# Kernel optimization log

Measured on AMD Instinct MI355X. Metric: run time of the kernel, lower is better.

Reference implementation:

```python
import jax, jax.numpy as jnp
import numpy as np

ALPHA = 0.01  # leaky_relu slope (forward default)

def _hist_entropy(x, bins):
    """Mean over batch of per-sample histogram entropy, matching
    np.histogram(sample, bins=bins) + entropy_calc(hist, bw=bins):
      H = -sum(p*log(p)) - log(1/bins) = -sum(p*log(p)) + log(bins).
    x: [B, D] float."""
    B, D = x.shape
    xmin = jnp.min(x, axis=1, keepdims=True)
    xmax = jnp.max(x, axis=1, keepdims=True)
    width = xmax - xmin
    safe_w = jnp.where(width > 0, width, 1.0)
    # np.histogram: equal-width bins over [min, max]; max value goes in last bin
    idx = jnp.floor((x - xmin) / safe_w * bins).astype(jnp.int32)
    idx = jnp.clip(idx, 0, bins - 1)
    flat = (jnp.arange(B, dtype=jnp.int32)[:, None] * bins + idx).reshape(-1)
    counts = jnp.zeros(B * bins, jnp.float32).at[flat].add(1.0).reshape(B, bins)
    p = counts / jnp.float32(D)
    plogp = jnp.where(p > 0, p * jnp.log(jnp.where(p > 0, p, 1.0)), 0.0)
    H = -jnp.sum(plogp, axis=1) + jnp.log(jnp.float32(bins))  # [B]
    return jnp.mean(H)

def _lin(x, W, b):
    return x @ W.T + b

def setup_inputs() -> dict:
    key = jax.random.key(0)
    ks = jax.random.split(key, 13)
    B = 65536
    dims = [(784, 256), (256, 128), (128, 128), (128, 128), (128, 32), (32, 10)]
    inp = {"x": jax.random.normal(ks[0], (B, 784), dtype=jnp.float32)}
    for i, (din, dout) in enumerate(dims):
        s = 1.0 / np.sqrt(din)
        inp[f"W{i+1}"] = jax.random.uniform(ks[1 + 2 * i], (dout, din), jnp.float32, -s, s)
        inp[f"b{i+1}"] = jax.random.uniform(ks[2 + 2 * i], (dout,), jnp.float32, -s, s)
    return inp

def reference(x, W1, b1, W2, b2, W3, b3, W4, b4, W5, b5, W6, b6):
    x = x.reshape(-1, 784)
    Hs = []
    for (W, b) in [(W1, b1), (W2, b2), (W3, b3), (W4, b4), (W5, b5)]:
        x = jax.nn.leaky_relu(_lin(x, W, b), ALPHA)
        Hs.append(_hist_entropy(x, x.shape[1]))  # bins = dim / bin_ratio(=1)
    x = jax.nn.relu(_lin(x, W6, b6))
    out = jax.nn.log_softmax(x, axis=1)
    return (out, Hs[0], Hs[1], Hs[2], Hs[3], Hs[4])
```

## Files before the change

### kernel.cpp

```cpp
#include <hip/hip_runtime.h>
#include <hip/hip_bf16.h>
#include <math.h>

#define ALPHA 0.01f

typedef __bf16 bf16x8 __attribute__((ext_vector_type(8)));
typedef float  floatx4 __attribute__((ext_vector_type(4)));

static __device__ __forceinline__ unsigned short f2bf_bits(float f) {
    return __builtin_bit_cast(unsigned short, (__bf16)f);
}

static __device__ __forceinline__ void glds16(const void* g, void* l) {
    __builtin_amdgcn_global_load_lds(
        (const __attribute__((address_space(1))) unsigned int*)g,
        (__attribute__((address_space(3))) unsigned int*)l, 16, 0, 0);
}

template <int CTRL>
static __device__ __forceinline__ float dppmov(float x) {
    int r = __builtin_amdgcn_update_dpp(0, __builtin_bit_cast(int, x), CTRL, 0xf, 0xf, false);
    return __builtin_bit_cast(float, r);
}
static __device__ __forceinline__ float red16min(float x) {
    x = fminf(x, dppmov<0x121>(x)); x = fminf(x, dppmov<0x122>(x));
    x = fminf(x, dppmov<0x124>(x)); x = fminf(x, dppmov<0x128>(x));
    return x;
}
static __device__ __forceinline__ float red16max(float x) {
    x = fmaxf(x, dppmov<0x121>(x)); x = fmaxf(x, dppmov<0x122>(x));
    x = fmaxf(x, dppmov<0x124>(x)); x = fmaxf(x, dppmov<0x128>(x));
    return x;
}
static __device__ __forceinline__ float red16sum(float x) {
    x += dppmov<0x121>(x); x += dppmov<0x122>(x);
    x += dppmov<0x124>(x); x += dppmov<0x128>(x);
    return x;
}

template <int DIN, int DOUT, bool XF32, bool WRES, int MINB>
__global__ __launch_bounds__(256, MINB) void layer_mfma(
    const void* __restrict__ Xin, const unsigned short* __restrict__ Wf,
    const float* __restrict__ bias, unsigned short* __restrict__ Y,
    float* __restrict__ Hpart)
{
    constexpr int CTN     = DOUT / 16;
    constexpr int KT_FULL = DIN / 32;
    constexpr int TAIL    = DIN % 32;
    constexpr int HALF    = DOUT / 2;
    constexpr int LOG2D   = (DOUT == 256) ? 8 : (DOUT == 128) ? 7 : 5;
    constexpr float LOGB  = (DOUT == 256) ? 5.54517744f
                          : (DOUT == 128) ? 4.85203026f : 3.46573590f;
    constexpr int XBYTES  = WRES ? 16 : 64 * 32 * (XF32 ? 4 : 2);
    constexpr int WBYTES  = WRES ? (size_t)DIN * DOUT * 2 : DOUT * 64;
    constexpr int WSLOTS  = (DIN / 32) * CTN * 64;
    static_assert(DOUT % 32 == 0 && DOUT <= 256, "DOUT");
    static_assert(XF32 || TAIL == 0, "bf16 input requires DIN%32==0");

    __shared__ __align__(16) char smemX[XBYTES];
    __shared__ __align__(16) char smemW[WBYTES];
    __shared__ unsigned int counts[16][HALF + 1];
    __shared__ float hsum[4];

    const int t      = threadIdx.x;
    const int lane   = t & 63;
    const int lane16 = lane & 15;
    const int q      = lane >> 4;
    const int w      = t >> 6;
    const int row0   = blockIdx.x * 64;
    const int myrow  = w * 16 + lane16;

    float biasr[CTN];
    #pragma unroll
    for (int ct = 0; ct < CTN; ct++) biasr[ct] = bias[ct * 16 + lane16];

    floatx4 acc[CTN];
    #pragma unroll
    for (int ct = 0; ct < CTN; ct++) acc[ct] = (floatx4)(0.0f);

    if constexpr (WRES) {
        static_assert(WSLOTS % 256 == 0, "WSLOTS");
        #pragma unroll
        for (int i = 0; i < WSLOTS / 256; i++)
            glds16(Wf + ((size_t)(i * 256 + w * 64 + lane)) * 8,
                   smemW + (i * 256 + w * 64) * 16);
        __syncthreads();

        const unsigned short* X = (const unsigned short*)Xin;
        const size_t abase = (size_t)(row0 + myrow) * DIN + q * 8;
        bf16x8 acur = *(const bf16x8*)(X + abase);
        #pragma unroll
        for (int kt = 0; kt < KT_FULL; kt++) {
            bf16x8 anxt = acur;
            if (kt + 1 < KT_FULL)
                anxt = *(const bf16x8*)(X + abase + (kt + 1) * 32);
            #pragma unroll
            for (int ct = 0; ct < CTN; ct++) {
                bf16x8 bw = *(const bf16x8*)(smemW + ((kt * CTN + ct) * 64 + lane) * 16);
                acc[ct] = __builtin_amdgcn_mfma_f32_16x16x32_bf16(acur, bw, acc[ct], 0, 0, 0);
            }
            acur = anxt;
        }
    } else {
        auto stageW = [&](int kt) {
            #pragma unroll
            for (int j = w; j < CTN; j += 4)
                glds16(Wf + ((size_t)kt * CTN * 64 + j * 64 + lane) * 8,
                       smemW + j * 64 * 16);
        };
        auto stageX = [&](int kt) {
            const float* X = (const float*)Xin;
            #pragma unroll
            for (int j = 0; j < 2; j++) {
                int s  = w * 128 + j * 64 + lane;
                int gc = (s & ~7) | ((s ^ (s >> 3)) & 7);
                int r  = gc >> 3, c = gc & 7;
                glds16(X + (size_t)(row0 + r) * DIN + kt * 32 + c * 4,
                       smemX + (w * 128 + j * 64) * 16);
            }
        };
        auto compute = [&]() {
            int s0 = myrow * 8 + (((2 * q)     ^ myrow) & 7);
            int s1 = myrow * 8 + (((2 * q + 1) ^ myrow) & 7);
            float4 f0 = *(const float4*)(smemX + s0 * 16);
            float4 f1 = *(const float4*)(smemX + s1 * 16);
            uint4 pk;
            pk.x = (unsigned)f2bf_bits(f0.x) | ((unsigned)f2bf_bits(f0.y) << 16);
            pk.y = (unsigned)f2bf_bits(f0.z) | ((unsigned)f2bf_bits(f0.w) << 16);
            pk.z = (unsigned)f2bf_bits(f1.x) | ((unsigned)f2bf_bits(f1.y) << 16);
            pk.w = (unsigned)f2bf_bits(f1.z) | ((unsigned)f2bf_bits(f1.w) << 16);
            bf16x8 a = __builtin_bit_cast(bf16x8, pk);
            #pragma unroll
            for (int ct = 0; ct < CTN; ct++) {
                bf16x8 bw = *(const bf16x8*)(smemW + (ct * 64 + lane) * 16);
                acc[ct] = __builtin_amdgcn_mfma_f32_16x16x32_bf16(a, bw, acc[ct], 0, 0, 0);
            }
        };

        #pragma unroll 1
        for (int kt = 0; kt < KT_FULL; kt++) {
            __syncthreads();
            stageX(kt);
            stageW(kt);
            __syncthreads();
            compute();
        }
        if constexpr (TAIL > 0) {
            __syncthreads();
            stageW(KT_FULL);
            {
                const float* X = (const float*)Xin;
                int r = t >> 2, c = t & 3;
                float4 v = *(const float4*)(X + (size_t)(row0 + r) * DIN
                                            + KT_FULL * 32 + c * 4);
                *(float4*)(smemX + (r * 8 + ((c ^ r) & 7)) * 16) = v;
                int c2 = c + 4;
                *(float4*)(smemX + (r * 8 + ((c2 ^ r) & 7)) * 16)
                    = make_float4(0.f, 0.f, 0.f, 0.f);
            }
            __syncthreads();
            compute();
        }
    }

    #pragma unroll
    for (int ct = 0; ct < CTN; ct++) {
        #pragma unroll
        for (int reg = 0; reg < 4; reg++) {
            float v = acc[ct][reg] + biasr[ct];
            v = v > 0.0f ? v : ALPHA * v;
            acc[ct][reg] = v;
            Y[(size_t)(row0 + w * 16 + q * 4 + reg) * DOUT
              + ct * 16 + lane16] = f2bf_bits(v);
        }
    }

    unsigned int* cc = counts[w * 4 + q];
    float Hq = 0.0f;
    #pragma unroll
    for (int reg = 0; reg < 4; reg++) {
        float mn = acc[0][reg], mx = mn;
        #pragma unroll
        for (int ct = 1; ct < CTN; ct++) {
            mn = fminf(mn, acc[ct][reg]);
            mx = fmaxf(mx, acc[ct][reg]);
        }
        mn = red16min(mn);
        mx = red16max(mx);
        float wdt = mx - mn;
        float scale = (float)DOUT / (wdt > 0.0f ? wdt : 1.0f);

        #pragma unroll
        for (int i = 0; i < DOUT / 32; i++) cc[lane16 + 16 * i] = 0u;

        #pragma unroll
        for (int ct = 0; ct < CTN; ct++) {
            int b = (int)((acc[ct][reg] - mn) * scale);
            b = b < (DOUT - 1) ? b : (DOUT - 1);
            atomicAdd(&cc[b & (HALF - 1)],
                      1u << (((b >> (LOG2D - 1)) & 1) << 4));
        }

        float s = 0.0f;
        #pragma unroll
        for (int i = 0; i < DOUT / 32; i++) {
            unsigned int word = cc[lane16 + 16 * i];
            int c0 = (int)(word & 0xffffu), c1 = (int)(word >> 16);
            if (c0 > 0) { float p = (float)c0 * (1.0f / (float)DOUT); s += p * __logf(p); }
            if (c1 > 0) { float p = (float)c1 * (1.0f / (float)DOUT); s += p * __logf(p); }
        }
        s = red16sum(s);
        Hq += LOGB - s;
    }
    Hq += __shfl_xor(Hq, 16, 64);
    Hq += __shfl_xor(Hq, 32, 64);

    if (lane == 0) hsum[w] = Hq;
    __syncthreads();
    if (t == 0) Hpart[blockIdx.x] = hsum[0] + hsum[1] + hsum[2] + hsum[3];
}

template <int DIN, int DOUT, bool AG>
static __device__ __forceinline__ float tail_layer(
    const unsigned short* __restrict__ Ag, size_t arow,
    char* __restrict__ yt,
    const unsigned short* __restrict__ Wf, const float* __restrict__ bias,
    unsigned int* __restrict__ cc, int lane)
{
    constexpr int KT  = DIN / 32, CTN = DOUT / 16;
    constexpr int NCI = DIN / 8,  NCO = DOUT / 8;
    constexpr int HALF  = DOUT / 2;
    constexpr int LOG2D = (DOUT == 128) ? 7 : 5;
    constexpr float LOGB = (DOUT == 128) ? 4.85203026f : 3.46573590f;
    const int lane16 = lane & 15, q = lane >> 4;

    bf16x8 a[KT];
    if constexpr (AG) {
        #pragma unroll
        for (int kt = 0; kt < KT; kt++)
            a[kt] = *(const bf16x8*)(Ag + arow + q * 8 + kt * 32);
    } else {
        asm volatile("s_waitcnt lgkmcnt(0)" ::: "memory");
        #pragma unroll
        for (int kt = 0; kt < KT; kt++) {
            int cs = (kt * 4 + q) ^ (lane16 & (NCI - 1));
            a[kt] = *(const bf16x8*)(yt + lane16 * (DIN * 2) + cs * 16);
        }
    }

    float biasr[CTN];
    #pragma unroll
    for (int ct = 0; ct < CTN; ct++) biasr[ct] = bias[ct * 16 + lane16];

    floatx4 acc[CTN];
    #pragma unroll
    for (int ct = 0; ct < CTN; ct++) acc[ct] = (floatx4)(0.0f);

    #pragma unroll
    for (int kt = 0; kt < KT; kt++) {
        #pragma unroll
        for (int ct = 0; ct < CTN; ct++) {
            bf16x8 bw = *(const bf16x8*)(Wf + ((size_t)(kt * CTN + ct) * 64 + lane) * 8);
            acc[ct] = __builtin_amdgcn_mfma_f32_16x16x32_bf16(a[kt], bw, acc[ct], 0, 0, 0);
        }
    }

    #pragma unroll
    for (int ct = 0; ct < CTN; ct++) {
        #pragma unroll
        for (int reg = 0; reg < 4; reg++) {
            float v = acc[ct][reg] + biasr[ct];
            v = v > 0.0f ? v : ALPHA * v;
            acc[ct][reg] = v;
            int r  = q * 4 + reg;
            int c  = (ct * 16 + lane16) >> 3;
            int cs = c ^ (r & (NCO - 1));
            *(unsigned short*)(yt + r * (DOUT * 2) + cs * 16 + (lane16 & 7) * 2)
                = f2bf_bits(v);
        }
    }

    float Hq = 0.0f;
    #pragma unroll
    for (int reg = 0; reg < 4; reg++) {
        float mn = acc[0][reg], mx = mn;
        #pragma unroll
        for (int ct = 1; ct < CTN; ct++) {
            mn = fminf(mn, acc[ct][reg]);
            mx = fmaxf(mx, acc[ct][reg]);
        }
        mn = red16min(mn);
        mx = red16max(mx);
        float wdt = mx - mn;
        float scale = (float)DOUT / (wdt > 0.0f ? wdt : 1.0f);

        #pragma unroll
        for (int i = 0; i < DOUT / 32; i++) cc[lane16 + 16 * i] = 0u;

        #pragma unroll
        for (int ct = 0; ct < CTN; ct++) {
            int b = (int)((acc[ct][reg] - mn) * scale);
            b = b < (DOUT - 1) ? b : (DOUT - 1);
            atomicAdd(&cc[b & (HALF - 1)],
                      1u << (((b >> (LOG2D - 1)) & 1) << 4));
        }

        float s = 0.0f;
        #pragma unroll
        for (int i = 0; i < DOUT / 32; i++) {
            unsigned int word = cc[lane16 + 16 * i];
            int c0 = (int)(word & 0xffffu), c1 = (int)(word >> 16);
            if (c0 > 0) { float p = (float)c0 * (1.0f / (float)DOUT); s += p * __logf(p); }
            if (c1 > 0) { float p = (float)c1 * (1.0f / (float)DOUT); s += p * __logf(p); }
        }
        s = red16sum(s);
        Hq += LOGB - s;
    }
    Hq += __shfl_xor(Hq, 16, 64);
    Hq += __shfl_xor(Hq, 32, 64);
    return Hq;
}

__global__ __launch_bounds__(256, 3) void tail_fused(
    const unsigned short* __restrict__ Xb,
    const unsigned short* __restrict__ W2f, const float* __restrict__ b2,
    const unsigned short* __restrict__ W3f, const float* __restrict__ b3,
    const unsigned short* __restrict__ W4f, const float* __restrict__ b4,
    const unsigned short* __restrict__ W5f, const float* __restrict__ b5,
    const float* __restrict__ W6, const float* __restrict__ b6,
    float* __restrict__ out, float* __restrict__ Hpart)
{
    __shared__ __align__(16) char yts[4][16 * 128 * 2];
    __shared__ unsigned int counts[16][65];

    const int t = threadIdx.x;
    const int lane = t & 63, lane16 = lane & 15, q = lane >> 4, w = t >> 6;
    char* yt = yts[w];
    unsigned int* cc = counts[w * 4 + q];
    const int row0 = blockIdx.x * 64 + w * 16;
    const size_t arow = (size_t)(row0 + lane16) * 256;
    const int hidx = blockIdx.x * 4 + w;

    float H;
    H = tail_layer<256, 128, true >(Xb, arow, yt, W2f, b2, cc, lane);
    if (lane == 0) Hpart[1 * 4096 + hidx] = H;
    H = tail_layer<128, 128, false>(Xb, 0, yt, W3f, b3, cc, lane);
    if (lane == 0) Hpart[2 * 4096 + hidx] = H;
    H = tail_layer<128, 128, false>(Xb, 0, yt, W4f, b4, cc, lane);
    if (lane == 0) Hpart[3 * 4096 + hidx] = H;
    H = tail_layer<128,  32, false>(Xb, 0, yt, W5f, b5, cc, lane);
    if (lane == 0) Hpart[4 * 4096 + hidx] = H;

    asm volatile("s_waitcnt lgkmcnt(0)" ::: "memory");
    float x[32];
    #pragma unroll
    for (int c = 0; c < 4; c++) {
        int cs = c ^ (lane16 & 3);
        bf16x8 v = *(const bf16x8*)(yt + lane16 * 64 + cs * 16);
        #pragma unroll
        for (int j = 0; j < 8; j++) x[c * 8 + j] = (float)v[j];
    }

    float z[3];
    float m = -1e30f;
    #pragma unroll
    for (int s2 = 0; s2 < 3; s2++) {
        int jj = q * 3 + s2;
        float a6 = 0.0f;
        if (jj < 10) {
            a6 = b6[jj];
            #pragma unroll
            for (int k = 0; k < 32; k++) a6 = fmaf(x[k], W6[jj * 32 + k], a6);
            a6 = fmaxf(a6, 0.0f);
            m = fmaxf(m, a6);
        }
        z[s2] = a6;
    }
    m = fmaxf(m, __shfl_xor(m, 16, 64));
    m = fmaxf(m, __shfl_xor(m, 32, 64));
    float se = 0.0f;
    #pragma unroll
    for (int s2 = 0; s2 < 3; s2++)
        if (q * 3 + s2 < 10) se += __expf(z[s2] - m);
    se += __shfl_xor(se, 16, 64);
    se += __shfl_xor(se, 32, 64);
    float ls = __logf(se);
    const size_t ro = (size_t)(row0 + lane16) * 10;
    #pragma unroll
    for (int s2 = 0; s2 < 3; s2++) {
        int jj = q * 3 + s2;
        if (jj < 10) out[ro + jj] = z[s2] - m - ls;
    }
}

__global__ void convert_wfrag(const float* __restrict__ W1, const float* __restrict__ W2,
                              const float* __restrict__ W3, const float* __restrict__ W4,
                              const float* __restrict__ W5, unsigned short* __restrict__ out)
{
    int s = blockIdx.x * 256 + threadIdx.x;
    if (s >= 34304) return;
    const float* W; int DIN, CTN, sl;
    if      (s < 25600) { W = W1; DIN = 784; CTN = 16; sl = s;         }
    else if (s < 29696) { W = W2; DIN = 256; CTN = 8;  sl = s - 25600; }
    else if (s < 31744) { W = W3; DIN = 128; CTN = 8;  sl = s - 29696; }
    else if (s < 33792) { W = W4; DIN = 128; CTN = 8;  sl = s - 31744; }
    else                { W = W5; DIN = 128; CTN = 2;  sl = s - 33792; }
    int kt = sl / (CTN * 64);
    int ct = (sl / 64) % CTN;
    int ln = sl & 63;
    int r  = ct * 16 + (ln & 15);
    int k0 = kt * 32 + (ln >> 4) * 8;
    unsigned short v[8];
    #pragma unroll
    for (int j = 0; j < 8; j++) {
        int k = k0 + j;
        v[j] = (k < DIN) ? f2bf_bits(W[(size_t)r * DIN + k]) : (unsigned short)0;
    }
    uint4 pk;
    pk.x = (unsigned)v[0] | ((unsigned)v[1] << 16);
    pk.y = (unsigned)v[2] | ((unsigned)v[3] << 16);
    pk.z = (unsigned)v[4] | ((unsigned)v[5] << 16);
    pk.w = (unsigned)v[6] | ((unsigned)v[7] << 16);
    *(uint4*)(out + (size_t)s * 8) = pk;
}

__global__ __launch_bounds__(256) void hreduce(const float* __restrict__ Hp,
                                               float* __restrict__ out_tail)
{
    __shared__ float sm[4];
    const int t = threadIdx.x, lane = t & 63, w = t >> 6;
    const int l = blockIdx.x;
    const int n = l ? 4096 : 1024;
    const float* p = Hp + (size_t)l * 4096;
    float s = 0.0f;
    for (int i = t; i < n; i += 256) s += p[i];
    #pragma unroll
    for (int off = 1; off <= 32; off <<= 1) s += __shfl_xor(s, off, 64);
    if (lane == 0) sm[w] = s;
    __syncthreads();
    if (t == 0)
        out_tail[l] = (sm[0] + sm[1] + sm[2] + sm[3]) * (1.0f / 65536.0f);
}

extern "C" void kernel_launch(void* const* d_in, const int* in_sizes, int n_in,
                              void* d_out, int out_size, void* d_ws, size_t ws_size,
                              hipStream_t stream)
{
    const float* x  = (const float*)d_in[0];
    const float* W1 = (const float*)d_in[1];  const float* b1 = (const float*)d_in[2];
    const float* W2 = (const float*)d_in[3];  const float* b2 = (const float*)d_in[4];
    const float* W3 = (const float*)d_in[5];  const float* b3 = (const float*)d_in[6];
    const float* W4 = (const float*)d_in[7];  const float* b4 = (const float*)d_in[8];
    const float* W5 = (const float*)d_in[9];  const float* b5 = (const float*)d_in[10];
    const float* W6 = (const float*)d_in[11]; const float* b6 = (const float*)d_in[12];
    float* out = (float*)d_out;

    constexpr int B = 65536;
    char* ws = (char*)d_ws;
    float* Hpart = (float*)ws;
    unsigned short* Wfrag = (unsigned short*)(ws + 81920);
    unsigned short* W1f = Wfrag;
    unsigned short* W2f = W1f + 25600 * 8;
    unsigned short* W3f = W2f + 4096 * 8;
    unsigned short* W4f = W3f + 2048 * 8;
    unsigned short* W5f = W4f + 2048 * 8;
    unsigned short* bufA = (unsigned short*)(ws + (1 << 20));

    convert_wfrag<<<134, 256, 0, stream>>>(W1, W2, W3, W4, W5, Wfrag);

    layer_mfma<784, 256, true, false, 4><<<B / 64, 256, 0, stream>>>(
        x, W1f, b1, bufA, Hpart);

    tail_fused<<<B / 64, 256, 0, stream>>>(
        bufA, W2f, b2, W3f, b3, W4f, b4, W5f, b5, W6, b6, out, Hpart);

    hreduce<<<5, 256, 0, stream>>>(Hpart, out + (size_t)B * 10);
}
```

Measured before the change: 408.4 us.

## Fuse layer-1 GEMM with tail layers into one mega kernel

Measured after the change: 401.6 us. About the same (-1.7%).

```diff
diff --git a/kernel.cpp b/kernel.cpp
--- a/kernel.cpp
+++ b/kernel.cpp
@@ -9,6 +9,9 @@
 
 static __device__ __forceinline__ unsigned short f2bf_bits(float f) {
     return __builtin_bit_cast(unsigned short, (__bf16)f);
+}
+static __device__ __forceinline__ float bf2f(unsigned short u) {
+    return __builtin_bit_cast(float, (unsigned)u << 16);
 }
 
 static __device__ __forceinline__ void glds16(const void* g, void* l) {
@@ -38,78 +41,146 @@
     return x;
 }
 
-template <int DIN, int DOUT, bool XF32, bool WRES, int MINB>
-__global__ __launch_bounds__(256, MINB) void layer_mfma(
-    const void* __restrict__ Xin, const unsigned short* __restrict__ Wf,
-    const float* __restrict__ bias, unsigned short* __restrict__ Y,
-    float* __restrict__ Hpart)
-{
-    constexpr int CTN     = DOUT / 16;
-    constexpr int KT_FULL = DIN / 32;
-    constexpr int TAIL    = DIN % 32;
-    constexpr int HALF    = DOUT / 2;
-    constexpr int LOG2D   = (DOUT == 256) ? 8 : (DOUT == 128) ? 7 : 5;
-    constexpr float LOGB  = (DOUT == 256) ? 5.54517744f
-                          : (DOUT == 128) ? 4.85203026f : 3.46573590f;
-    constexpr int XBYTES  = WRES ? 16 : 64 * 32 * (XF32 ? 4 : 2);
-    constexpr int WBYTES  = WRES ? (size_t)DIN * DOUT * 2 : DOUT * 64;
-    constexpr int WSLOTS  = (DIN / 32) * CTN * 64;
-    static_assert(DOUT % 32 == 0 && DOUT <= 256, "DOUT");
-    static_assert(XF32 || TAIL == 0, "bf16 input requires DIN%32==0");
-
-    __shared__ __align__(16) char smemX[XBYTES];
-    __shared__ __align__(16) char smemW[WBYTES];
-    __shared__ unsigned int counts[16][HALF + 1];
+template <int DOUT>
+static __device__ __forceinline__ float entropy_tile(const floatx4* acc,
+        unsigned int* cc, int lane16)
+{
+    constexpr int CTN   = DOUT / 16;
+    constexpr int HALF  = DOUT / 2;
+    constexpr int LOG2D = (DOUT == 256) ? 8 : (DOUT == 128) ? 7 : 5;
+    constexpr float LOGB = (DOUT == 256) ? 5.54517744f
+                         : (DOUT == 128) ? 4.85203026f : 3.46573590f;
+    float Hq = 0.0f;
+    #pragma unroll
+    for (int reg = 0; reg < 4; reg++) {
+        float mn = acc[0][reg], mx = mn;
+        #pragma unroll
+        for (int ct = 1; ct < CTN; ct++) {
+            mn = fminf(mn, acc[ct][reg]);
+            mx = fmaxf(mx, acc[ct][reg]);
+        }
+        mn = red16min(mn);
+        mx = red16max(mx);
+        float wdt = mx - mn;
+        float scale = (float)DOUT / (wdt > 0.0f ? wdt : 1.0f);
+
+        #pragma unroll
+        for (int i = 0; i < DOUT / 32; i++) cc[lane16 + 16 * i] = 0u;
+
+        #pragma unroll
+        for (int ct = 0; ct < CTN; ct++) {
+            int b = (int)((acc[ct][reg] - mn) * scale);
+            b = b < (DOUT - 1) ? b : (DOUT - 1);
+            atomicAdd(&cc[b & (HALF - 1)],
+                      1u << (((b >> (LOG2D - 1)) & 1) << 4));
+        }
+
+        float s = 0.0f;
+        #pragma unroll
+        for (int i = 0; i < DOUT / 32; i++) {
+            unsigned int word = cc[lane16 + 16 * i];
+            int c0 = (int)(word & 0xffffu), c1 = (int)(word >> 16);
+            if (c0 > 0) { float p = (float)c0 * (1.0f / (float)DOUT); s += p * __logf(p); }
+            if (c1 > 0) { float p = (float)c1 * (1.0f / (float)DOUT); s += p * __logf(p); }
+        }
+        s = red16sum(s);
+        Hq += LOGB - s;
+    }
+    Hq += __shfl_xor(Hq, 16, 64);
+    Hq += __shfl_xor(Hq, 32, 64);
+    return Hq;
+}
+
+template <int DIN, int DOUT>
+static __device__ __forceinline__ float tail_layer(const bf16x8* a,
+    char* __restrict__ yt,
+    const unsigned short* __restrict__ Wf, const float* __restrict__ bias,
+    unsigned int* __restrict__ cc, int lane)
+{
+    constexpr int KT = DIN / 32, CTN = DOUT / 16, NCO = DOUT / 8;
+    const int lane16 = lane & 15, q = lane >> 4;
+
+    floatx4 acc[CTN];
+    #pragma unroll
+    for (int ct = 0; ct < CTN; ct++) acc[ct] = (floatx4)(0.0f);
+
+    #pragma unroll
+    for (int kt = 0; kt < KT; kt++) {
+        #pragma unroll
+        for (int ct = 0; ct < CTN; ct++) {
+            bf16x8 bw = *(const bf16x8*)(Wf + ((size_t)(kt * CTN + ct) * 64 + lane) * 8);
+            acc[ct] = __builtin_amdgcn_mfma_f32_16x16x32_bf16(a[kt], bw, acc[ct], 0, 0, 0);
+        }
+    }
+
+    #pragma unroll
+    for (int ct = 0; ct < CTN; ct++) {
+        float bb = bias[ct * 16 + lane16];
+        #pragma unroll
+        for (int reg = 0; reg < 4; reg++) {
+            float v = acc[ct][reg] + bb;
+            v = v > 0.0f ? v : ALPHA * v;
+            acc[ct][reg] = v;
+            int r  = q * 4 + reg;
+            int c  = (ct * 16 + lane16) >> 3;
+            int cs = c ^ (r & (NCO - 1));
+            *(unsigned short*)(yt + r * (DOUT * 2) + cs * 16 + (lane16 & 7) * 2)
+                = f2bf_bits(v);
+        }
+    }
+    return entropy_tile<DOUT>(acc, cc, lane16);
+}
+
+template <int DIN>
+static __device__ __forceinline__ void load_afrags(bf16x8* a,
+    const char* __restrict__ yt, int lane16, int q)
+{
+    constexpr int KT = DIN / 32, NCI = DIN / 8;
+    asm volatile("s_waitcnt lgkmcnt(0)" ::: "memory");
+    #pragma unroll
+    for (int kt = 0; kt < KT; kt++) {
+        int cs = (kt * 4 + q) ^ (lane16 & (NCI - 1));
+        a[kt] = *(const bf16x8*)(yt + lane16 * (DIN * 2) + cs * 16);
+    }
+    asm volatile("s_waitcnt lgkmcnt(0)" ::: "memory");
+}
+
+__global__ __launch_bounds__(256, 4) void mega(
+    const float* __restrict__ X,
+    const unsigned short* __restrict__ W1f, const float* __restrict__ b1,
+    const unsigned short* __restrict__ W2f, const float* __restrict__ b2,
+    const unsigned short* __restrict__ W3f, const float* __restrict__ b3,
+    const unsigned short* __restrict__ W4f, const float* __restrict__ b4,
+    const unsigned short* __restrict__ W5f, const float* __restrict__ b5,
+    const float* __restrict__ W6, const float* __restrict__ b6,
+    float* __restrict__ out, float* __restrict__ Hpart)
+{
+    __shared__ __align__(16) char regA[24576];
+    __shared__ unsigned int cnt[16][129];
     __shared__ float hsum[4];
 
-    const int t      = threadIdx.x;
-    const int lane   = t & 63;
-    const int lane16 = lane & 15;
-    const int q      = lane >> 4;
-    const int w      = t >> 6;
-    const int row0   = blockIdx.x * 64;
-    const int myrow  = w * 16 + lane16;
-
-    float biasr[CTN];
-    #pragma unroll
-    for (int ct = 0; ct < CTN; ct++) biasr[ct] = bias[ct * 16 + lane16];
-
-    floatx4 acc[CTN];
-    #pragma unroll
-    for (int ct = 0; ct < CTN; ct++) acc[ct] = (floatx4)(0.0f);
-
-    if constexpr (WRES) {
-        static_assert(WSLOTS % 256 == 0, "WSLOTS");
-        #pragma unroll
-        for (int i = 0; i < WSLOTS / 256; i++)
-            glds16(Wf + ((size_t)(i * 256 + w * 64 + lane)) * 8,
-                   smemW + (i * 256 + w * 64) * 16);
-        __syncthreads();
-
-        const unsigned short* X = (const unsigned short*)Xin;
-        const size_t abase = (size_t)(row0 + myrow) * DIN + q * 8;
-        bf16x8 acur = *(const bf16x8*)(X + abase);
-        #pragma unroll
-        for (int kt = 0; kt < KT_FULL; kt++) {
-            bf16x8 anxt = acur;
-            if (kt + 1 < KT_FULL)
-                anxt = *(const bf16x8*)(X + abase + (kt + 1) * 32);
-            #pragma unroll
-            for (int ct = 0; ct < CTN; ct++) {
-                bf16x8 bw = *(const bf16x8*)(smemW + ((kt * CTN + ct) * 64 + lane) * 16);
-                acc[ct] = __builtin_amdgcn_mfma_f32_16x16x32_bf16(acur, bw, acc[ct], 0, 0, 0);
-            }
-            acur = anxt;
-        }
-    } else {
+    const int t = threadIdx.x;
+    const int lane = t & 63, lane16 = lane & 15, q = lane >> 4, w = t >> 6;
+    const int row0 = blockIdx.x * 64;
+    const int myrow = w * 16 + lane16;
+    unsigned int* cc = cnt[w * 4 + q];
+    char* yt = regA + w * 4096;
+
+    floatx4 acc1[16];
+    #pragma unroll
+    for (int ct = 0; ct < 16; ct++) acc1[ct] = (floatx4)(0.0f);
+    {
+        constexpr int DIN = 784, CTN = 16, KT_FULL = 24;
+        char* smemX = regA;
+        char* smemW = regA + 8192;
+
         auto stageW = [&](int kt) {
             #pragma unroll
             for (int j = w; j < CTN; j += 4)
-                glds16(Wf + ((size_t)kt * CTN * 64 + j * 64 + lane) * 8,
+                glds16(W1f + ((size_t)kt * CTN * 64 + j * 64 + lane) * 8,
                        smemW + j * 64 * 16);
         };
         auto stageX = [&](int kt) {
-            const float* X = (const float*)Xin;
             #pragma unroll
             for (int j = 0; j < 2; j++) {
                 int s  = w * 128 + j * 64 + lane;
@@ -133,7 +204,7 @@
             #pragma unroll
             for (int ct = 0; ct < CTN; ct++) {
                 bf16x8 bw = *(const bf16x8*)(smemW + (ct * 64 + lane) * 16);
-                acc[ct] = __builtin_amdgcn_mfma_f32_16x16x32_bf16(a, bw, acc[ct], 0, 0, 0);
+                acc1[ct] = __builtin_amdgcn_mfma_f32_16x16x32_bf16(a, bw, acc1[ct], 0, 0, 0);
             }
         };
 
@@ -145,220 +216,83 @@
             __syncthreads();
             compute();
         }
-        if constexpr (TAIL > 0) {
-            __syncthreads();
-            stageW(KT_FULL);
-            {
-                const float* X = (const float*)Xin;
-                int r = t >> 2, c = t & 3;
-                float4 v = *(const float4*)(X + (size_t)(row0 + r) * DIN
-                                            + KT_FULL * 32 + c * 4);
-                *(float4*)(smemX + (r * 8 + ((c ^ r) & 7)) * 16) = v;
-                int c2 = c + 4;
-                *(float4*)(smemX + (r * 8 + ((c2 ^ r) & 7)) * 16)
-                    = make_float4(0.f, 0.f, 0.f, 0.f);
-            }
-            __syncthreads();
-            compute();
-        }
-    }
-
-    #pragma unroll
-    for (int ct = 0; ct < CTN; ct++) {
+        __syncthreads();
+        stageW(KT_FULL);
+        {
+            int r = t >> 2, c = t & 3;
+            float4 v = *(const float4*)(X + (size_t)(row0 + r) * DIN
+                                        + KT_FULL * 32 + c * 4);
+            *(float4*)(smemX + (r * 8 + ((c ^ r) & 7)) * 16) = v;
+            int c2 = c + 4;
+            *(float4*)(smemX + (r * 8 + ((c2 ^ r) & 7)) * 16)
+                = make_float4(0.f, 0.f, 0.f, 0.f);
+        }
+        __syncthreads();
+        compute();
+    }
+
+    #pragma unroll
+    for (int ct = 0; ct < 16; ct++) {
+        float bb = b1[ct * 16 + lane16];
         #pragma unroll
         for (int reg = 0; reg < 4; reg++) {
-            float v = acc[ct][reg] + biasr[ct];
-            v = v > 0.0f ? v : ALPHA * v;
-            acc[ct][reg] = v;
-            Y[(size_t)(row0 + w * 16 + q * 4 + reg) * DOUT
-              + ct * 16 + lane16] = f2bf_bits(v);
-        }
-    }
-
-    unsigned int* cc = counts[w * 4 + q];
-    float Hq = 0.0f;
-    #pragma unroll
-    for (int reg = 0; reg < 4; reg++) {
-        float mn = acc[0][reg], mx = mn;
-        #pragma unroll
-        for (int ct = 1; ct < CTN; ct++) {
-            mn = fminf(mn, acc[ct][reg]);
-            mx = fmaxf(mx, acc[ct][reg]);
-        }
-        mn = red16min(mn);
-        mx = red16max(mx);
-        float wdt = mx - mn;
-        float scale = (float)DOUT / (wdt > 0.0f ? wdt : 1.0f);
-
-        #pragma unroll
-        for (int i = 0; i < DOUT / 32; i++) cc[lane16 + 16 * i] = 0u;
-
-        #pragma unroll
-        for (int ct = 0; ct < CTN; ct++) {
-            int b = (int)((acc[ct][reg] - mn) * scale);
-            b = b < (DOUT - 1) ? b : (DOUT - 1);
-            atomicAdd(&cc[b & (HALF - 1)],
-                      1u << (((b >> (LOG2D - 1)) & 1) << 4));
-        }
-
-        float s = 0.0f;
-        #pragma unroll
-        for (int i = 0; i < DOUT / 32; i++) {
-            unsigned int word = cc[lane16 + 16 * i];
-            int c0 = (int)(word & 0xffffu), c1 = (int)(word >> 16);
-            if (c0 > 0) { float p = (float)c0 * (1.0f / (float)DOUT); s += p * __logf(p); }
-            if (c1 > 0) { float p = (float)c1 * (1.0f / (float)DOUT); s += p * __logf(p); }
-        }
-        s = red16sum(s);
-        Hq += LOGB - s;
-    }
-    Hq += __shfl_xor(Hq, 16, 64);
-    Hq += __shfl_xor(Hq, 32, 64);
-
-    if (lane == 0) hsum[w] = Hq;
+            float v = acc1[ct][reg] + bb;
+            acc1[ct][reg] = v > 0.0f ? v : ALPHA * v;
+        }
+    }
+
+    float H1 = entropy_tile<256>(acc1, cc, lane16);
+    if (lane == 0) hsum[w] = H1;
     __syncthreads();
     if (t == 0) Hpart[blockIdx.x] = hsum[0] + hsum[1] + hsum[2] + hsum[3];
-}
-
-template <int DIN, int DOUT, bool AG>
-static __device__ __forceinline__ float tail_layer(
-    const unsigned short* __restrict__ Ag, size_t arow,
-    char* __restrict__ yt,
-    const unsigned short* __restrict__ Wf, const float* __restrict__ bias,
-    unsigned int* __restrict__ cc, int lane)
-{
-    constexpr int KT  = DIN / 32, CTN = DOUT / 16;
-    constexpr int NCI = DIN / 8,  NCO = DOUT / 8;
-    constexpr int HALF  = DOUT / 2;
-    constexpr int LOG2D = (DOUT == 128) ? 7 : 5;
-    constexpr float LOGB = (DOUT == 128) ? 4.85203026f : 3.46573590f;
-    const int lane16 = lane & 15, q = lane >> 4;
-
-    bf16x8 a[KT];
-    if constexpr (AG) {
-        #pragma unroll
-        for (int kt = 0; kt < KT; kt++)
-            a[kt] = *(const bf16x8*)(Ag + arow + q * 8 + kt * 32);
-    } else {
+
+    bf16x8 a2[8];
+    #pragma unroll
+    for (int p = 0; p < 2; p++) {
+        #pragma unroll
+        for (int ct = 0; ct < 8; ct++) {
+            #pragma unroll
+            for (int reg = 0; reg < 4; reg++) {
+                int r  = q * 4 + reg;
+                int c  = (ct * 16 + lane16) >> 3;
+                int cs = c ^ r;
+                *(unsigned short*)(yt + r * 256 + cs * 16 + (lane16 & 7) * 2)
+                    = f2bf_bits(acc1[p * 8 + ct][reg]);
+            }
+        }
         asm volatile("s_waitcnt lgkmcnt(0)" ::: "memory");
         #pragma unroll
-        for (int kt = 0; kt < KT; kt++) {
-            int cs = (kt * 4 + q) ^ (lane16 & (NCI - 1));
-            a[kt] = *(const bf16x8*)(yt + lane16 * (DIN * 2) + cs * 16);
-        }
-    }
-
-    float biasr[CTN];
-    #pragma unroll
-    for (int ct = 0; ct < CTN; ct++) biasr[ct] = bias[ct * 16 + lane16];
-
-    floatx4 acc[CTN];
-    #pragma unroll
-    for (int ct = 0; ct < CTN; ct++) acc[ct] = (floatx4)(0.0f);
-
-    #pragma unroll
-    for (int kt = 0; kt < KT; kt++) {
-        #pragma unroll
-        for (int ct = 0; ct < CTN; ct++) {
-            bf16x8 bw = *(const bf16x8*)(Wf + ((size_t)(kt * CTN + ct) * 64 + lane) * 8);
-            acc[ct] = __builtin_amdgcn_mfma_f32_16x16x32_bf16(a[kt], bw, acc[ct], 0, 0, 0);
-        }
-    }
-
-    #pragma unroll
-    for (int ct = 0; ct < CTN; ct++) {
-        #pragma unroll
-        for (int reg = 0; reg < 4; reg++) {
-            float v = acc[ct][reg] + biasr[ct];
-            v = v > 0.0f ? v : ALPHA * v;
-            acc[ct][reg] = v;
-            int r  = q * 4 + reg;
-            int c  = (ct * 16 + lane16) >> 3;
-            int cs = c ^ (r & (NCO - 1));
-            *(unsigned short*)(yt + r * (DOUT * 2) + cs * 16 + (lane16 & 7) * 2)
-                = f2bf_bits(v);
-        }
-    }
-
-    float Hq = 0.0f;
-    #pragma unroll
-    for (int reg = 0; reg < 4; reg++) {
-        float mn = acc[0][reg], mx = mn;
-        #pragma unroll
-        for (int ct = 1; ct < CTN; ct++) {
-            mn = fminf(mn, acc[ct][reg]);
-            mx = fmaxf(mx, acc[ct][reg]);
-        }
-        mn = red16min(mn);
-        mx = red16max(mx);
-        float wdt = mx - mn;
-        float scale = (float)DOUT / (wdt > 0.0f ? wdt : 1.0f);
-
-        #pragma unroll
-        for (int i = 0; i < DOUT / 32; i++) cc[lane16 + 16 * i] = 0u;
-
-        #pragma unroll
-        for (int ct = 0; ct < CTN; ct++) {
-            int b = (int)((acc[ct][reg] - mn) * scale);
-            b = b < (DOUT - 1) ? b : (DOUT - 1);
-            atomicAdd(&cc[b & (HALF - 1)],
-                      1u << (((b >> (LOG2D - 1)) & 1) << 4));
-        }
-
-        float s = 0.0f;
-        #pragma unroll
-        for (int i = 0; i < DOUT / 32; i++) {
-            unsigned int word = cc[lane16 + 16 * i];
-            int c0 = (int)(word & 0xffffu), c1 = (int)(word >> 16);
-            if (c0 > 0) { float p = (float)c0 * (1.0f / (float)DOUT); s += p * __logf(p); }
-            if (c1 > 0) { float p = (float)c1 * (1.0f / (float)DOUT); s += p * __logf(p); }
-        }
-        s = red16sum(s);
-        Hq += LOGB - s;
-    }
-    Hq += __shfl_xor(Hq, 16, 64);
-    Hq += __shfl_xor(Hq, 32, 64);
-    return Hq;
-}
-
-__global__ __launch_bounds__(256, 3) void tail_fused(
-    const unsigned short* __restrict__ Xb,
-    const unsigned short* __restrict__ W2f, const float* __restrict__ b2,
-    const unsigned short* __restrict__ W3f, const float* __restrict__ b3,
-    const unsigned short* __restrict__ W4f, const float* __restrict__ b4,
-    const unsigned short* __restrict__ W5f, const float* __restrict__ b5,
-    const float* __restrict__ W6, const float* __restrict__ b6,
-    float* __restrict__ out, float* __restrict__ Hpart)
-{
-    __shared__ __align__(16) char yts[4][16 * 128 * 2];
-    __shared__ unsigned int counts[16][65];
-
-    const int t = threadIdx.x;
-    const int lane = t & 63, lane16 = lane & 15, q = lane >> 4, w = t >> 6;
-    char* yt = yts[w];
-    unsigned int* cc = counts[w * 4 + q];
-    const int row0 = blockIdx.x * 64 + w * 16;
-    const size_t arow = (size_t)(row0 + lane16) * 256;
-    const int hidx = blockIdx.x * 4 + w;
-
-    float H;
-    H = tail_layer<256, 128, true >(Xb, arow, yt, W2f, b2, cc, lane);
-    if (lane == 0) Hpart[1 * 4096 + hidx] = H;
-    H = tail_layer<128, 128, false>(Xb, 0, yt, W3f, b3, cc, lane);
-    if (lane == 0) Hpart[2 * 4096 + hidx] = H;
-    H = tail_layer<128, 128, false>(Xb, 0, yt, W4f, b4, cc, lane);
-    if (lane == 0) Hpart[3 * 4096 + hidx] = H;
-    H = tail_layer<128,  32, false>(Xb, 0, yt, W5f, b5, cc, lane);
-    if (lane == 0) Hpart[4 * 4096 + hidx] = H;
+        for (int kt = 0; kt < 4; kt++) {
+            int cs = (kt * 4 + q) ^ lane16;
+            a2[p * 4 + kt] = *(const bf16x8*)(yt + lane16 * 256 + cs * 16);
+        }
+        asm volatile("s_waitcnt lgkmcnt(0)" ::: "memory");
+    }
+
+    float H = tail_layer<256, 128>(a2, yt, W2f, b2, cc, lane);
+    if (lane == 0) Hpart[1 * 4096 + blockIdx.x * 4 + w] = H;
+
+    bf16x8 a[4];
+    load_afrags<128>(a, yt, lane16, q);
+    H = tail_layer<128, 128>(a, yt, W3f, b3, cc, lane);
+    if (lane == 0) Hpart[2 * 4096 + blockIdx.x * 4 + w] = H;
+
+    load_afrags<128>(a, yt, lane16, q);
+    H = tail_layer<128, 128>(a, yt, W4f, b4, cc, lane);
+    if (lane == 0) Hpart[3 * 4096 + blockIdx.x * 4 + w] = H;
+
+    load_afrags<128>(a, yt, lane16, q);
+    H = tail_layer<128, 32>(a, yt, W5f, b5, cc, lane);
+    if (lane == 0) Hpart[4 * 4096 + blockIdx.x * 4 + w] = H;
 
     asm volatile("s_waitcnt lgkmcnt(0)" ::: "memory");
-    float x[32];
+    float x6[32];
     #pragma unroll
     for (int c = 0; c < 4; c++) {
         int cs = c ^ (lane16 & 3);
         bf16x8 v = *(const bf16x8*)(yt + lane16 * 64 + cs * 16);
         #pragma unroll
-        for (int j = 0; j < 8; j++) x[c * 8 + j] = (float)v[j];
+        for (int j = 0; j < 8; j++) x6[c * 8 + j] = (float)v[j];
     }
 
     float z[3];
@@ -370,7 +304,7 @@
         if (jj < 10) {
             a6 = b6[jj];
             #pragma unroll
-            for (int k = 0; k < 32; k++) a6 = fmaf(x[k], W6[jj * 32 + k], a6);
+            for (int k = 0; k < 32; k++) a6 = fmaf(x6[k], W6[jj * 32 + k], a6);
             a6 = fmaxf(a6, 0.0f);
             m = fmaxf(m, a6);
         }
@@ -385,7 +319,7 @@
     se += __shfl_xor(se, 16, 64);
     se += __shfl_xor(se, 32, 64);
     float ls = __logf(se);
-    const size_t ro = (size_t)(row0 + lane16) * 10;
+    const size_t ro = (size_t)(row0 + w * 16 + lane16) * 10;
     #pragma unroll
     for (int s2 = 0; s2 < 3; s2++) {
         int jj = q * 3 + s2;
@@ -464,15 +398,11 @@
     unsigned short* W3f = W2f + 4096 * 8;
     unsigned short* W4f = W3f + 2048 * 8;
     unsigned short* W5f = W4f + 2048 * 8;
-    unsigned short* bufA = (unsigned short*)(ws + (1 << 20));
 
     convert_wfrag<<<134, 256, 0, stream>>>(W1, W2, W3, W4, W5, Wfrag);
 
-    layer_mfma<784, 256, true, false, 4><<<B / 64, 256, 0, stream>>>(
-        x, W1f, b1, bufA, Hpart);
-
-    tail_fused<<<B / 64, 256, 0, stream>>>(
-        bufA, W2f, b2, W3f, b3, W4f, b4, W5f, b5, W6, b6, out, Hpart);
+    mega<<<B / 64, 256, 0, stream>>>(
+        x, W1f, b1, W2f, b2, W3f, b3, W4f, b4, W5f, b5, W6, b6, out, Hpart);
 
     hreduce<<<5, 256, 0, stream>>>(Hpart, out + (size_t)B * 10);
 }
```
